# Optimization experiments

Hardware: AMD Instinct MI355X
Metric: run time of the kernel (lower is better)

The kernel has to match this reference:

```python
import jax, jax.numpy as jnp
import numpy as np
import math

B, S, D = 16, 577, 768          # batch, seq (24*24 grid + 1 cls), in_dim=att_dim
H, HD = 12, 64                  # heads, head_dim
GRID = 24                       # height = width; S = GRID*GRID + rpe_skip
RATIO = 1.9
ALPHA, BETA, GAMMA = 1.0 * RATIO, 2.0 * RATIO, 8.0 * RATIO
BETA_INT = int(BETA)            # 3
NUM_BUCKETS = (2 * BETA_INT + 1) ** 2 + 1  # 49 product buckets + 1 extra for skip (cls) = 50


def _piecewise_index(d):
    # iRPE piecewise bucket index (numpy, static). d: integer offsets.
    d = d.astype(np.float64)
    ad = np.abs(d)
    log_part = ALPHA + np.log(np.maximum(ad, 1e-9) / ALPHA) / math.log(GAMMA / ALPHA) * (BETA - ALPHA)
    y_out = np.sign(d) * np.clip(np.round(log_part), None, BETA)
    idx = np.where(ad <= ALPHA, np.round(d), y_out)
    return np.trunc(idx).astype(np.int64)  # torch .to(int) truncates toward zero


def make_rp_bucket():
    # 2D 'product' method bucket ids with skip=1 (cls token -> extra bucket)
    ii, jj = np.meshgrid(np.arange(GRID), np.arange(GRID), indexing='ij')
    pos = np.stack([ii.ravel(), jj.ravel()], axis=-1)          # (L,2)
    diff = pos[:, None, :] - pos[None, :, :]                    # (L,L,2)
    Sb = 2 * BETA_INT + 1
    r = _piecewise_index(diff[..., 0]) + BETA_INT               # [0, 2*beta_int]
    c = _piecewise_index(diff[..., 1]) + BETA_INT
    pid = r * Sb + c                                            # [0, 48]
    L = GRID * GRID
    bucket = np.full((L + 1, L + 1), NUM_BUCKETS - 1, dtype=np.int32)
    bucket[1:, 1:] = pid
    return jnp.asarray(bucket)


def setup_inputs() -> dict:
    key = jax.random.key(0)
    k1, k2, k3 = jax.random.split(key, 3)
    x = jax.random.normal(k1, (B, S, D), dtype=jnp.float32)
    w_qkv = jax.random.normal(k2, (3 * D, D), dtype=jnp.float32) * 0.02   # torch Linear weight (out,in)
    rpe_table = jax.random.normal(k3, (HD, NUM_BUCKETS), dtype=jnp.float32) * 0.02  # shared-head contextual table
    rp_bucket = make_rp_bucket()                                # (S,S) int32
    return {"x": x, "w_qkv": w_qkv, "rpe_table": rpe_table, "rp_bucket": rp_bucket}


def reference(x, w_qkv, rpe_table, rp_bucket):
    qkv = x @ w_qkv.T                                           # (B,S,3D)
    q, k, v = jnp.split(qkv, 3, axis=-1)
    # Faithful to torch source: plain reshape (B,S,D)->(B,H,S,HD) (no transpose-split)
    scale = 1.0 / jnp.sqrt(jnp.asarray(HD, x.dtype))
    q = q.reshape(B, H, S, HD) * scale
    k = k.reshape(B, H, S, HD)
    v = v.reshape(B, H, S, HD)
    qk = jnp.einsum('bhid,bhjd->bhij', q, k)                    # (B,H,S,S)
    # contextual rpe_k: bias[b,h,i,j] = (q[b,h,i] . rpe_table[:, rp_bucket[i,j]])
    ctx = jnp.einsum('bhid,dc->bhic', q, rpe_table)             # (B,H,S,NUM_BUCKETS)
    idx = jnp.broadcast_to(rp_bucket[None, None].astype(jnp.int32), (B, H, S, S))
    bias = jnp.take_along_axis(ctx, idx, axis=-1)               # (B,H,S,S)
    att = jax.nn.softmax(qk + bias, axis=-1)
    out = jnp.einsum('bhij,bhjd->bhid', att, v)                 # (B,H,S,HD)
    y = out.transpose(0, 2, 1, 3).reshape(B, S, D)              # out_proj is Identity (out_dim==att_dim)
    return y
```

## Files before the change

### kernel.cpp

```cpp
#include <hip/hip_runtime.h>

constexpr int BN_  = 16;
constexpr int SN_  = 577;
constexpr int SP_  = 640;
constexpr int DN_  = 768;
constexpr int HN_  = 12;
constexpr int HD_  = 64;
constexpr int NB_  = 50;
constexpr int MR_  = BN_ * SN_;
constexpr int MRP_ = 73 * 128;
constexpr int NQ_  = 3 * DN_;
constexpr int BHS_ = BN_ * HN_ * SN_;
constexpr int SHD_ = SN_ * HD_;

constexpr int NBX_ = MRP_ * DN_ / 2048;
constexpr int NBW_ = NQ_ * DN_ / 2048;
constexpr int NRPX_ = 5 * 4 * 2 * 10 * 4 * 64;
constexpr int NBRX_ = NRPX_ / 256;

typedef __attribute__((ext_vector_type(8))) short short8;
typedef __attribute__((ext_vector_type(4))) float f32x4;

__device__ __forceinline__ short f2bf(float f) {
  union { float f; unsigned u; } v; v.f = f;
  unsigned r = (v.u + 0x7fffu + ((v.u >> 16) & 1u)) >> 16;
  return (short)r;
}

__device__ __forceinline__ float ex2(float x) {
  float r; asm("v_exp_f32 %0, %1" : "=v"(r) : "v"(x)); return r;
}

__device__ __forceinline__ unsigned cvtpk(float a, float b) {
  unsigned r; asm("v_cvt_pk_bf16_f32 %0, %1, %2" : "=v"(r) : "v"(a), "v"(b));
  return r;
}

__device__ __forceinline__ float bf2f(unsigned short u) {
  union { unsigned u; float f; } v; v.u = ((unsigned)u) << 16; return v.f;
}

__device__ __forceinline__ void gload16(const void* g, void* l) {
  __builtin_amdgcn_global_load_lds(
      (const __attribute__((address_space(1))) unsigned int*)g,
      (__attribute__((address_space(3))) unsigned int*)l, 16, 0, 0);
}

__launch_bounds__(256)
__global__ void prep_k(const float* __restrict__ x, short* __restrict__ xb,
                       const float* __restrict__ w, short* __restrict__ wb,
                       const int* __restrict__ rpb, unsigned* __restrict__ rpbX) {
  const int bid = blockIdx.x;
  const int t = threadIdx.x;
  if (bid < NBX_ + NBW_) {
    const float* src; short* dst; int n_src, i;
    if (bid < NBX_) { src = x; dst = xb; n_src = MR_ * DN_; i = (bid * 256 + t) * 8; }
    else { src = w; dst = wb; n_src = NQ_ * DN_; i = ((bid - NBX_) * 256 + t) * 8; }
    union { short8 v; short u[8]; } pk;
    if (i < n_src) {
      const float4 a = *(const float4*)(src + i);
      const float4 b = *(const float4*)(src + i + 4);
      pk.u[0] = f2bf(a.x); pk.u[1] = f2bf(a.y); pk.u[2] = f2bf(a.z); pk.u[3] = f2bf(a.w);
      pk.u[4] = f2bf(b.x); pk.u[5] = f2bf(b.y); pk.u[6] = f2bf(b.z); pk.u[7] = f2bf(b.w);
    } else {
#pragma unroll
      for (int j = 0; j < 8; ++j) pk.u[j] = 0;
    }
    *(short8*)(dst + i) = pk.v;
  } else {
    const int idx = (bid - NBX_ - NBW_) * 256 + t;
    if (idx >= NRPX_) return;
    const int lane = idx & 63, chunk = idx >> 6;
    const int nt = chunk & 3;
    const int jt = (chunk >> 2) % 10;
    const int rest = chunk / 40;
    const int s  = rest & 1;
    const int w4 = (rest >> 1) & 3;
    const int qt = rest >> 3;
    const int g = lane >> 4, ln = lane & 15;
    int row = qt * 128 + w4 * 32 + s * 16 + ln;
    if (row > SN_ - 1) row = SN_ - 1;
    const int j0 = jt * 64 + nt * 16 + 4 * g;
    union { unsigned u; uchar4 c; } pk;
    pk.c.x = (j0     < SN_) ? (unsigned char)rpb[row * SN_ + j0    ] : 0;
    pk.c.y = (j0 + 1 < SN_) ? (unsigned char)rpb[row * SN_ + j0 + 1] : 0;
    pk.c.z = (j0 + 2 < SN_) ? (unsigned char)rpb[row * SN_ + j0 + 2] : 0;
    pk.c.w = (j0 + 3 < SN_) ? (unsigned char)rpb[row * SN_ + j0 + 3] : 0;
    rpbX[idx] = pk.u;
  }
}

__launch_bounds__(256)
__global__ void qkv_mfma_k(const short* __restrict__ xb, const short* __restrict__ wb,
                           short* __restrict__ Qbf, short* __restrict__ Ksw,
                           short* __restrict__ Vbf) {
  __shared__ short SB[32768];
  const int t = threadIdx.x;
  const int w = t >> 6, lane = t & 63, g = lane >> 4, ln = lane & 15;
  const int wm = w >> 1, wn = w & 1;
  const int m0 = blockIdx.y * 128, n0 = blockIdx.x * 128;

  const int rlo = lane >> 3;
  const int gu  = (lane & 7) ^ rlo;
  const short* ga[4]; const short* gb[4];
  int lOff[4];
#pragma unroll
  for (int q = 0; q < 4; ++q) {
    const int rl = w * 32 + q * 8 + rlo;
    ga[q] = xb + (size_t)(m0 + rl) * DN_ + gu * 8;
    gb[q] = wb + (size_t)(n0 + rl) * DN_ + gu * 8;
    lOff[q] = w * 2048 + q * 512;
  }

  f32x4 acc[4][4];
#pragma unroll
  for (int mt = 0; mt < 4; ++mt)
#pragma unroll
    for (int nt = 0; nt < 4; ++nt) acc[mt][nt] = (f32x4){0.f, 0.f, 0.f, 0.f};

#pragma unroll
  for (int q = 0; q < 4; ++q) {
    gload16(ga[q], SB + lOff[q]);
    gload16(gb[q], SB + 16384 + lOff[q]);
  }
  __syncthreads();

  int cur = 0;
  for (int k0 = 0; k0 < DN_; k0 += 64) {
    if (k0 + 64 < DN_) {
      const int nb = (cur ^ 1) * 8192;
#pragma unroll
      for (int q = 0; q < 4; ++q) {
        gload16(ga[q] + k0 + 64, SB + nb + lOff[q]);
        gload16(gb[q] + k0 + 64, SB + 16384 + nb + lOff[q]);
      }
    }
    const short* Ac = SB + cur * 8192;
    const short* Bc = SB + 16384 + cur * 8192;
#pragma unroll
    for (int kc = 0; kc < 2; ++kc) {
      short8 af[4], bf[4];
#pragma unroll
      for (int mt = 0; mt < 4; ++mt) {
        const int row = wm * 64 + mt * 16 + ln;
        const int u = (kc * 4 + g) ^ (row & 7);
        af[mt] = *(const short8*)&Ac[row * 64 + u * 8];
      }
#pragma unroll
      for (int nt = 0; nt < 4; ++nt) {
        const int row = wn * 64 + nt * 16 + ln;
        const int u = (kc * 4 + g) ^ (row & 7);
        bf[nt] = *(const short8*)&Bc[row * 64 + u * 8];
      }
#pragma unroll
      for (int mt = 0; mt < 4; ++mt)
#pragma unroll
        for (int nt = 0; nt < 4; ++nt)
          acc[mt][nt] = __builtin_amdgcn_mfma_f32_16x16x32_bf16(af[mt], bf[nt], acc[mt][nt], 0, 0, 0);
    }
    __syncthreads();
    cur ^= 1;
  }

  const int wbase = w * 4608;
  const int nw0  = n0 + wn * 64;
  const int secg = nw0 / DN_;
  const int cbw  = nw0 - secg * DN_;
  const float QSC = 0.18033688011112042f;
#pragma unroll
  for (int mt = 0; mt < 4; ++mt)
#pragma unroll
    for (int nt = 0; nt < 4; ++nt)
#pragma unroll
      for (int r = 0; r < 4; ++r) {
        float v = acc[mt][nt][r];
        if (secg == 0) v *= QSC;
        SB[wbase + (mt * 16 + 4 * g + r) * 72 + nt * 16 + ln] = f2bf(v);
      }
  const int gm = m0 + wm * 64 + lane;
  if (gm < MR_) {
    const int bb = gm / SN_;
    const int ss = gm - bb * SN_;
    const int pr = ss * DN_ + cbw;
    const int hh = pr / SHD_;
    const int ii = (pr - hh * SHD_) >> 6;
    const size_t ro = (size_t)(bb * HN_ + hh);
    const short* src = SB + wbase + lane * 72;
    if (secg == 0) {
      short* dst = Qbf + (ro * SN_ + ii) * 64;
#pragma unroll
      for (int u = 0; u < 8; ++u)
        *(short8*)(dst + u * 8) = *(const short8*)(src + u * 8);
    } else if (secg == 1) {
      short* dst = Ksw + (ro * SP_ + ii) * 64;
      const int sw = ii & 7;
#pragma unroll
      for (int u = 0; u < 8; ++u)
        *(short8*)(dst + (u ^ sw) * 8) = *(const short8*)(src + u * 8);
    } else {
      short* dst = Vbf + (ro * SP_ + ii) * 64;
#pragma unroll
      for (int u = 0; u < 8; ++u)
        *(short8*)(dst + u * 8) = *(const short8*)(src + u * 8);
    }
  }
}

__launch_bounds__(256)
__global__ void vtr_k(const short* __restrict__ Vbf, short* __restrict__ Vtsw) {
  __shared__ short T[64][72];
  const int t = threadIdx.x;
  const int jt = blockIdx.x, bh = blockIdx.y;
  const int j0 = jt * 64;
  {
    const int r = t >> 2, c0 = (t & 3) * 16;
    const short* src = Vbf + ((size_t)bh * SP_ + j0 + r) * 64 + c0;
    *(short8*)&T[r][c0]     = *(const short8*)(src);
    *(short8*)&T[r][c0 + 8] = *(const short8*)(src + 8);
  }
  __syncthreads();
  const int d = t >> 2;
  short* dst = Vtsw + ((size_t)bh * 64 + d) * SP_;
  const int sw = (d & 7) << 3;
#pragma unroll
  for (int e = 0; e < 4; ++e) {
    const int jl = (t & 3) * 16 + e * 4;
    const int jg = j0 + jl;
    short4 v;
    v.x = (jg + 0 < SN_) ? T[jl + 0][d] : (short)0;
    v.y = (jg + 1 < SN_) ? T[jl + 1][d] : (short)0;
    v.z = (jg + 2 < SN_) ? T[jl + 2][d] : (short)0;
    v.w = (jg + 3 < SN_) ? T[jl + 3][d] : (short)0;
    const int oq = (jg >> 2) & 7;
    const int pq = ((oq & 3) << 1) | (oq >> 2);
    const int p  = (jg & ~31) | (pq << 2);
    *(short4*)&dst[p ^ sw] = v;
  }
}

__launch_bounds__(256)
__global__ void attn_k(const short* __restrict__ Qbf, const short* __restrict__ Ksw,
                       const short* __restrict__ Vtsw, const float* __restrict__ rpe,
                       const unsigned* __restrict__ rpbX, float* __restrict__ y) {
  __shared__ short Kt[4096];
  __shared__ short Vt[4096];
  __shared__ unsigned short ctxs[4][32][53];
  short (*Rp)[64] = (short (*)[64])ctxs;

  const int t = threadIdx.x;
  const int w = t >> 6, lane = t & 63, g = lane >> 4, ln = lane & 15;
  const int wg = blockIdx.x;
  const int xcd = wg & 7, idx = wg >> 3;
  const int qt = idx % 5;
  const int bh = (idx / 5) * 8 + xcd;
  const int b = bh / HN_, h = bh - b * HN_;
  const int i0 = qt * 128;
  const size_t rb = (size_t)bh * SN_;
  const short* Kbh = Ksw + (size_t)bh * SP_ * 64;
  const short* Vbh = Vtsw + (size_t)bh * 64 * SP_;

  const int tK = t * 8;
  const int vRow = t >> 3, vCol = (t & 7) * 8;

  const unsigned* rpB = rpbX + qt * 20480 + w * 5120 + lane;

  short8 kr0, kr1, vr0, vr1;
  kr0 = *(const short8*)(Kbh + tK);
  kr1 = *(const short8*)(Kbh + 2048 + tK);
  vr0 = *(const short8*)(Vbh + (size_t)vRow * SP_ + vCol);
  vr1 = *(const short8*)(Vbh + (size_t)(32 + vRow) * SP_ + vCol);

  for (int e = t; e < 64 * 64; e += 256) {
    const int c = e >> 6, d = e & 63;
    Rp[c][d] = (c < NB_) ? f2bf(rpe[d * NB_ + c]) : (short)0;
  }

  short8 qf[2][2];
#pragma unroll
  for (int s = 0; s < 2; ++s) {
    int row = i0 + 32 * w + 16 * s + ln; if (row > SN_ - 1) row = SN_ - 1;
    const short* qp = Qbf + (rb + row) * 64;
    qf[s][0] = *(const short8*)(qp + 8 * g);
    qf[s][1] = *(const short8*)(qp + 32 + 8 * g);
  }

  __syncthreads();

  f32x4 accC[2][4];
#pragma unroll
  for (int s = 0; s < 2; ++s)
#pragma unroll
    for (int ct = 0; ct < 4; ++ct) accC[s][ct] = (f32x4){0.f, 0.f, 0.f, 0.f};
#pragma unroll
  for (int kc = 0; kc < 2; ++kc) {
#pragma unroll
    for (int ct = 0; ct < 4; ++ct) {
      const short8 rf = *(const short8*)&Rp[ct * 16 + ln][kc * 32 + 8 * g];
      accC[0][ct] = __builtin_amdgcn_mfma_f32_16x16x32_bf16(qf[0][kc], rf, accC[0][ct], 0, 0, 0);
      accC[1][ct] = __builtin_amdgcn_mfma_f32_16x16x32_bf16(qf[1][kc], rf, accC[1][ct], 0, 0, 0);
    }
  }
  __syncthreads();

#pragma unroll
  for (int s = 0; s < 2; ++s)
#pragma unroll
    for (int ct = 0; ct < 4; ++ct) {
      const int c = ct * 16 + ln;
      if (c < 53) {
#pragma unroll
        for (int r = 0; r < 4; ++r)
          ctxs[w][16 * s + 4 * g + r][c] = (unsigned short)f2bf(accC[s][ct][r]);
      }
    }

  float m0s = -3e38f, m1s = -3e38f, l0s = 0.f, l1s = 0.f;
  f32x4 accO[2][4];
#pragma unroll
  for (int s = 0; s < 2; ++s)
#pragma unroll
    for (int dt = 0; dt < 4; ++dt) accO[s][dt] = (f32x4){0.f, 0.f, 0.f, 0.f};

  const int swv = (ln & 7) << 3;

  for (int jt = 0; jt < 10; ++jt) {
    __syncthreads();
    *(short8*)&Kt[tK]        = kr0;
    *(short8*)&Kt[2048 + tK] = kr1;
    *(short8*)&Vt[tK]        = vr0;
    *(short8*)&Vt[2048 + tK] = vr1;
    __syncthreads();

    unsigned rpg[2][4];
#pragma unroll
    for (int s = 0; s < 2; ++s)
#pragma unroll
      for (int nt = 0; nt < 4; ++nt)
        rpg[s][nt] = rpB[s * 2560 + jt * 256 + nt * 64];

    if (jt < 9) {
      const int jn = jt * 64 + 64;
      kr0 = *(const short8*)(Kbh + (size_t)jn * 64 + tK);
      kr1 = *(const short8*)(Kbh + (size_t)jn * 64 + 2048 + tK);
      vr0 = *(const short8*)(Vbh + (size_t)vRow * SP_ + jn + vCol);
      vr1 = *(const short8*)(Vbh + (size_t)(32 + vRow) * SP_ + jn + vCol);
    }

    f32x4 accS[2][4];
#pragma unroll
    for (int s = 0; s < 2; ++s)
#pragma unroll
      for (int nt = 0; nt < 4; ++nt) accS[s][nt] = (f32x4){0.f, 0.f, 0.f, 0.f};
    __builtin_amdgcn_s_setprio(1);
#pragma unroll
    for (int kc = 0; kc < 2; ++kc) {
      const int cb = (kc * 32 + 8 * g) ^ swv;
#pragma unroll
      for (int nt = 0; nt < 4; ++nt) {
        const short8 kf = *(const short8*)&Kt[(nt * 16 + ln) * 64 + cb];
        accS[0][nt] = __builtin_amdgcn_mfma_f32_16x16x32_bf16(kf, qf[0][kc], accS[0][nt], 0, 0, 0);
        accS[1][nt] = __builtin_amdgcn_mfma_f32_16x16x32_bf16(kf, qf[1][kc], accS[1][nt], 0, 0, 0);
      }
    }
    __builtin_amdgcn_s_setprio(0);

    short8 pf[2][2];
#pragma unroll
    for (int s = 0; s < 2; ++s) {
      const unsigned short* cbase = &ctxs[w][16 * s + ln][0];
      float pv[4][4];
#pragma unroll
      for (int nt = 0; nt < 4; ++nt) {
        union { unsigned u; uchar4 c; } bk; bk.u = rpg[s][nt];
        pv[nt][0] = accS[s][nt][0] + bf2f(cbase[bk.c.x]);
        pv[nt][1] = accS[s][nt][1] + bf2f(cbase[bk.c.y]);
        pv[nt][2] = accS[s][nt][2] + bf2f(cbase[bk.c.z]);
        pv[nt][3] = accS[s][nt][3] + bf2f(cbase[bk.c.w]);
      }
      if (jt == 9) {
#pragma unroll
        for (int nt = 0; nt < 4; ++nt) {
          const int jb = jt * 64 + nt * 16 + 4 * g;
#pragma unroll
          for (int r = 0; r < 4; ++r)
            if (jb + r >= SN_) pv[nt][r] = -3e38f;
        }
      }

      float& m = (s == 0) ? m0s : m1s;
      float& l = (s == 0) ? l0s : l1s;

      float mq[4];
#pragma unroll
      for (int nt = 0; nt < 4; ++nt)
        mq[nt] = fmaxf(fmaxf(pv[nt][0], pv[nt][1]), fmaxf(pv[nt][2], pv[nt][3]));
      float mx = fmaxf(fmaxf(mq[0], mq[1]), fmaxf(mq[2], mq[3]));
      mx = fmaxf(mx, __shfl_xor(mx, 16));
      mx = fmaxf(mx, __shfl_xor(mx, 32));

      if (__any(mx > m + 8.f)) {
        const float mnew = fmaxf(m, mx);
        const float sc = ex2(m - mnew);
        float scr[4];
#pragma unroll
        for (int r = 0; r < 4; ++r) scr[r] = __shfl(sc, 4 * g + r);
#pragma unroll
        for (int dt = 0; dt < 4; ++dt)
#pragma unroll
          for (int r = 0; r < 4; ++r) accO[s][dt][r] *= scr[r];
        l *= sc;
        m = mnew;
      }

#pragma unroll
      for (int nt = 0; nt < 4; ++nt)
#pragma unroll
        for (int r = 0; r < 4; ++r)
          pv[nt][r] = ex2(pv[nt][r] - m);
      float sq[4];
#pragma unroll
      for (int nt = 0; nt < 4; ++nt)
        sq[nt] = (pv[nt][0] + pv[nt][1]) + (pv[nt][2] + pv[nt][3]);
      float sum = (sq[0] + sq[1]) + (sq[2] + sq[3]);
      sum += __shfl_xor(sum, 16);
      sum += __shfl_xor(sum, 32);
      l += sum;

#pragma unroll
      for (int kc = 0; kc < 2; ++kc) {
        union { short8 v; unsigned wd[4]; } pk;
        pk.wd[0] = cvtpk(pv[2 * kc][0],     pv[2 * kc][1]);
        pk.wd[1] = cvtpk(pv[2 * kc][2],     pv[2 * kc][3]);
        pk.wd[2] = cvtpk(pv[2 * kc + 1][0], pv[2 * kc + 1][1]);
        pk.wd[3] = cvtpk(pv[2 * kc + 1][2], pv[2 * kc + 1][3]);
        pf[s][kc] = pk.v;
      }
    }

    __builtin_amdgcn_s_setprio(1);
#pragma unroll
    for (int kc = 0; kc < 2; ++kc) {
      const int cb = (kc * 32 + 8 * g) ^ swv;
#pragma unroll
      for (int dt = 0; dt < 4; ++dt) {
        const short8 vf = *(const short8*)&Vt[(dt * 16 + ln) * 64 + cb];
        accO[0][dt] = __builtin_amdgcn_mfma_f32_16x16x32_bf16(pf[0][kc], vf, accO[0][dt], 0, 0, 0);
        accO[1][dt] = __builtin_amdgcn_mfma_f32_16x16x32_bf16(pf[1][kc], vf, accO[1][dt], 0, 0, 0);
      }
    }
    __builtin_amdgcn_s_setprio(0);
  }

#pragma unroll
  for (int s = 0; s < 2; ++s) {
    const float lv = (s == 0) ? l0s : l1s;
    float linv[4];
#pragma unroll
    for (int r = 0; r < 4; ++r) linv[r] = 1.f / __shfl(lv, 4 * g + r);
#pragma unroll
    for (int r = 0; r < 4; ++r) {
      const int i = i0 + 32 * w + 16 * s + 4 * g + r;
      if (i >= SN_) continue;
      float* yp = y + ((size_t)b * SN_ + i) * DN_ + h * HD_ + ln;
#pragma unroll
      for (int dt = 0; dt < 4; ++dt) yp[dt * 16] = accO[s][dt][r] * linv[r];
    }
  }
}

extern "C" void kernel_launch(void* const* d_in, const int* in_sizes, int n_in,
                              void* d_out, int out_size, void* d_ws, size_t ws_size,
                              hipStream_t stream) {
  const float* x   = (const float*)d_in[0];
  const float* w   = (const float*)d_in[1];
  const float* rpe = (const float*)d_in[2];
  const int*   rpb = (const int*)d_in[3];
  float* y = (float*)d_out;

  short* xb   = (short*)d_ws;
  short* wb   = xb + (size_t)MRP_ * DN_;
  short* Qbf  = wb + (size_t)NQ_ * DN_;
  short* Ksw  = Qbf + (size_t)BHS_ * HD_;
  short* Vbf  = Ksw + (size_t)BN_ * HN_ * SP_ * 64;
  short* Vtsw = Vbf + (size_t)BN_ * HN_ * SP_ * 64;
  unsigned* rpbX = (unsigned*)(Vtsw + (size_t)BN_ * HN_ * 64 * SP_);

  prep_k<<<dim3(NBX_ + NBW_ + NBRX_), 256, 0, stream>>>(x, xb, w, wb, rpb, rpbX);
  qkv_mfma_k<<<dim3(18, 73), 256, 0, stream>>>(xb, wb, Qbf, Ksw, Vbf);
  vtr_k<<<dim3(10, BN_ * HN_), 256, 0, stream>>>(Vbf, Vtsw);
  attn_k<<<dim3(960), 256, 0, stream>>>(Qbf, Ksw, Vtsw, rpe, rpbX, y);
}
```

Before: 139.9 us.

## Double-buffer K/V tiles in LDS using direct global-to-LDS loads

Replaces register-staged K/V tile loads (global to registers, then registers to LDS between two barriers) with direct global-to-LDS loads (`gload16`) into a double-buffered LDS area. The next tile is prefetched into the alternate buffer while the current one is used for the QK and PV MFMAs, with a single barrier per iteration. The aim is to drop the register round-trip and one barrier per tile and to overlap loads with compute. In exchange it doubles K/V LDS use, which may lower occupancy. Because the end-of-loop barrier likely waits for the outstanding prefetch, the achievable overlap is limited.

Result: no change. 141.5 us (+1.1%).

```diff
diff --git a/kernel.cpp b/kernel.cpp
--- a/kernel.cpp
+++ b/kernel.cpp
@@ -242,8 +242,8 @@
 __global__ void attn_k(const short* __restrict__ Qbf, const short* __restrict__ Ksw,
                        const short* __restrict__ Vtsw, const float* __restrict__ rpe,
                        const unsigned* __restrict__ rpbX, float* __restrict__ y) {
-  __shared__ short Kt[4096];
-  __shared__ short Vt[4096];
+  __shared__ short Kt[2 * 4096];
+  __shared__ short Vt[2 * 4096];
   __shared__ unsigned short ctxs[4][32][53];
   short (*Rp)[64] = (short (*)[64])ctxs;
 
@@ -259,16 +259,17 @@
   const short* Kbh = Ksw + (size_t)bh * SP_ * 64;
   const short* Vbh = Vtsw + (size_t)bh * 64 * SP_;
 
-  const int tK = t * 8;
-  const int vRow = t >> 3, vCol = (t & 7) * 8;
+  const int srow = w * 16 + (lane >> 3);
+  const int scol = (lane & 7) * 8;
+  const int sdst = w * 1024 + lane * 8;
 
   const unsigned* rpB = rpbX + qt * 20480 + w * 5120 + lane;
 
-  short8 kr0, kr1, vr0, vr1;
-  kr0 = *(const short8*)(Kbh + tK);
-  kr1 = *(const short8*)(Kbh + 2048 + tK);
-  vr0 = *(const short8*)(Vbh + (size_t)vRow * SP_ + vCol);
-  vr1 = *(const short8*)(Vbh + (size_t)(32 + vRow) * SP_ + vCol);
+#pragma unroll
+  for (int q = 0; q < 2; ++q) {
+    gload16(Kbh + (size_t)(srow + q * 8) * 64 + scol, Kt + sdst + q * 512);
+    gload16(Vbh + (size_t)(srow + q * 8) * SP_ + scol, Vt + sdst + q * 512);
+  }
 
   for (int e = t; e < 64 * 64; e += 256) {
     const int c = e >> 6, d = e & 63;
@@ -323,13 +324,17 @@
 
   const int swv = (ln & 7) << 3;
 
+  int cur = 0;
   for (int jt = 0; jt < 10; ++jt) {
-    __syncthreads();
-    *(short8*)&Kt[tK]        = kr0;
-    *(short8*)&Kt[2048 + tK] = kr1;
-    *(short8*)&Vt[tK]        = vr0;
-    *(short8*)&Vt[2048 + tK] = vr1;
-    __syncthreads();
+    if (jt < 9) {
+      const int jn = (jt + 1) * 64;
+      const int db = (cur ^ 1) * 4096;
+#pragma unroll
+      for (int q = 0; q < 2; ++q) {
+        gload16(Kbh + (size_t)(jn + srow + q * 8) * 64 + scol, Kt + db + sdst + q * 512);
+        gload16(Vbh + (size_t)(srow + q * 8) * SP_ + jn + scol, Vt + db + sdst + q * 512);
+      }
+    }
 
     unsigned rpg[2][4];
 #pragma unroll
@@ -338,13 +343,8 @@
       for (int nt = 0; nt < 4; ++nt)
         rpg[s][nt] = rpB[s * 2560 + jt * 256 + nt * 64];
 
-    if (jt < 9) {
-      const int jn = jt * 64 + 64;
-      kr0 = *(const short8*)(Kbh + (size_t)jn * 64 + tK);
-      kr1 = *(const short8*)(Kbh + (size_t)jn * 64 + 2048 + tK);
-      vr0 = *(const short8*)(Vbh + (size_t)vRow * SP_ + jn + vCol);
-      vr1 = *(const short8*)(Vbh + (size_t)(32 + vRow) * SP_ + jn + vCol);
-    }
+    const short* KtC = Kt + cur * 4096;
+    const short* VtC = Vt + cur * 4096;
 
     f32x4 accS[2][4];
 #pragma unroll
@@ -357,7 +357,7 @@
       const int cb = (kc * 32 + 8 * g) ^ swv;
 #pragma unroll
       for (int nt = 0; nt < 4; ++nt) {
-        const short8 kf = *(const short8*)&Kt[(nt * 16 + ln) * 64 + cb];
+        const short8 kf = *(const short8*)&KtC[(nt * 16 + ln) * 64 + cb];
         accS[0][nt] = __builtin_amdgcn_mfma_f32_16x16x32_bf16(kf, qf[0][kc], accS[0][nt], 0, 0, 0);
         accS[1][nt] = __builtin_amdgcn_mfma_f32_16x16x32_bf16(kf, qf[1][kc], accS[1][nt], 0, 0, 0);
       }
@@ -443,12 +443,15 @@
       const int cb = (kc * 32 + 8 * g) ^ swv;
 #pragma unroll
       for (int dt = 0; dt < 4; ++dt) {
-        const short8 vf = *(const short8*)&Vt[(dt * 16 + ln) * 64 + cb];
+        const short8 vf = *(const short8*)&VtC[(dt * 16 + ln) * 64 + cb];
         accO[0][dt] = __builtin_amdgcn_mfma_f32_16x16x32_bf16(pf[0][kc], vf, accO[0][dt], 0, 0, 0);
         accO[1][dt] = __builtin_amdgcn_mfma_f32_16x16x32_bf16(pf[1][kc], vf, accO[1][dt], 0, 0, 0);
       }
     }
     __builtin_amdgcn_s_setprio(0);
+
+    __syncthreads();
+    cur ^= 1;
   }
 
 #pragma unroll
```
